# Performance work log

Hardware: AMD Instinct MI355X
Metric: run time of the kernel (lower is better)

## Reference

```python
import jax, jax.numpy as jnp
import numpy as np

N_ITERS = 21
TEMPERATURE = 0.04


def setup_inputs() -> dict:
    key = jax.random.key(0)
    input_tensor = jax.random.normal(key, (4096, 128, 128), dtype=jnp.float32)
    return {"input_tensor": input_tensor}


def reference(input_tensor) -> jnp.ndarray:
    n = input_tensor.shape[1]
    log_alpha = input_tensor.reshape((-1, n, n)) / TEMPERATURE

    def body(_, la):
        la = la - jax.nn.logsumexp(la, axis=2, keepdims=True)  # row normalize
        la = la - jax.nn.logsumexp(la, axis=1, keepdims=True)  # col normalize
        return la

    log_alpha = jax.lax.fori_loop(0, N_ITERS, body, log_alpha)
    return jnp.exp(log_alpha)
```

## Files before the change

### kernel.cpp

```cpp
#include <hip/hip_runtime.h>

typedef short bf16x8 __attribute__((ext_vector_type(8)));
typedef float f32x4 __attribute__((ext_vector_type(4)));
typedef unsigned int u32;
typedef unsigned short u16;

#define NIT 21
#define SMIN 1e-38f
#define CSH  140.0f
#define LDSCOL 136

static __device__ __forceinline__ u16 f2bf(float f) {
    u32 u = __float_as_uint(f);
    u = (u + 0x7fffu + ((u >> 16) & 1u)) >> 16;
    return (u16)u;
}
static __device__ __forceinline__ float bf2f(u16 h) {
    return __uint_as_float(((u32)h) << 16);
}

__global__ void __attribute__((amdgpu_flat_work_group_size(256, 256),
                               amdgpu_waves_per_eu(4, 4)))
sinkhorn_kernel(const float* __restrict__ in, float* __restrict__ out) {
    const int t  = threadIdx.x;
    const int w  = t >> 6;
    const int lg = (t >> 4) & 3;
    const int ln = t & 15;
    const size_t mat = (size_t)blockIdx.x << 14;
    const float S = 36.067376022224085f;

    __shared__ __align__(16) u16 Ecm[128 * LDSCOL];
    __shared__ __align__(16) u16 a_lds[128];
    __shared__ __align__(16) u16 b_lds[128];

    bf16x8 af[2][4];

#pragma unroll
    for (int th = 0; th < 2; ++th) {
        const int M = w * 32 + th * 16 + ln;
        const float* src = in + mat + (size_t)M * 128 + lg * 8;
        const int ms = M ^ (lg << 4);
        float s = 0.f;
#pragma unroll
        for (int c = 0; c < 4; ++c) {
            float4 f0 = *(const float4*)(src + c * 32);
            float4 f1 = *(const float4*)(src + c * 32 + 4);
            float e0 = __builtin_amdgcn_exp2f(fmaf(f0.x, S, -CSH));
            float e1 = __builtin_amdgcn_exp2f(fmaf(f0.y, S, -CSH));
            float e2 = __builtin_amdgcn_exp2f(fmaf(f0.z, S, -CSH));
            float e3 = __builtin_amdgcn_exp2f(fmaf(f0.w, S, -CSH));
            float e4 = __builtin_amdgcn_exp2f(fmaf(f1.x, S, -CSH));
            float e5 = __builtin_amdgcn_exp2f(fmaf(f1.y, S, -CSH));
            float e6 = __builtin_amdgcn_exp2f(fmaf(f1.z, S, -CSH));
            float e7 = __builtin_amdgcn_exp2f(fmaf(f1.w, S, -CSH));
            s += ((e0 + e1) + (e2 + e3)) + ((e4 + e5) + (e6 + e7));
            bf16x8 fr;
            fr[0] = (short)f2bf(e0); fr[1] = (short)f2bf(e1);
            fr[2] = (short)f2bf(e2); fr[3] = (short)f2bf(e3);
            fr[4] = (short)f2bf(e4); fr[5] = (short)f2bf(e5);
            fr[6] = (short)f2bf(e6); fr[7] = (short)f2bf(e7);
            af[th][c] = fr;
            const int nb = c * 32 + lg * 8;
#pragma unroll
            for (int j = 0; j < 8; ++j)
                Ecm[(nb + j) * LDSCOL + ms] = (u16)fr[j];
        }
        s += __shfl_xor(s, 16);
        s += __shfl_xor(s, 32);
        if (lg == 0) a_lds[M] = f2bf(__builtin_amdgcn_rcpf(fmaxf(s, SMIN)));
    }
    __syncthreads();

    const f32x4 z4 = {0.f, 0.f, 0.f, 0.f};

#pragma unroll 1
    for (int it = 0; it < NIT; ++it) {
        f32x4 acc0 = z4, acc1 = z4;
        const int N0 = w * 32 + ln;
        const int k0s = ((N0 >> 3) & 3) << 4;
        const int k1s = (((N0 + 16) >> 3) & 3) << 4;
#pragma unroll
        for (int c = 0; c < 4; ++c) {
            const int kb = c * 32 + lg * 8;
            bf16x8 aop = *(const bf16x8*)&a_lds[kb];
            bf16x8 b0  = *(const bf16x8*)&Ecm[N0 * LDSCOL + (kb ^ k0s)];
            bf16x8 b1  = *(const bf16x8*)&Ecm[(N0 + 16) * LDSCOL + (kb ^ k1s)];
            acc0 = __builtin_amdgcn_mfma_f32_16x16x32_bf16(aop, b0, acc0, 0, 0, 0);
            acc1 = __builtin_amdgcn_mfma_f32_16x16x32_bf16(aop, b1, acc1, 0, 0, 0);
        }
        if (lg == 0) {
            b_lds[w * 32 + ln]      = f2bf(__builtin_amdgcn_rcpf(fmaxf(acc0[0], SMIN)));
            b_lds[w * 32 + 16 + ln] = f2bf(__builtin_amdgcn_rcpf(fmaxf(acc1[0], SMIN)));
        }
        __syncthreads();

        if (it < NIT - 1) {
            f32x4 r0 = z4, r1 = z4;
#pragma unroll
            for (int c = 0; c < 4; ++c) {
                bf16x8 bop = *(const bf16x8*)&b_lds[c * 32 + lg * 8];
                r0 = __builtin_amdgcn_mfma_f32_16x16x32_bf16(af[0][c], bop, r0, 0, 0, 0);
                r1 = __builtin_amdgcn_mfma_f32_16x16x32_bf16(af[1][c], bop, r1, 0, 0, 0);
            }
            if (ln == 0) {
#pragma unroll
                for (int r = 0; r < 4; ++r) {
                    a_lds[w * 32 +      lg * 4 + r] = f2bf(__builtin_amdgcn_rcpf(fmaxf(r0[r], SMIN)));
                    a_lds[w * 32 + 16 + lg * 4 + r] = f2bf(__builtin_amdgcn_rcpf(fmaxf(r1[r], SMIN)));
                }
            }
            __syncthreads();
        }
    }

#pragma unroll
    for (int th = 0; th < 2; ++th) {
        const int M = w * 32 + th * 16 + ln;
        float* dst = out + mat + (size_t)M * 128 + lg * 8;
        const float av = bf2f(a_lds[M]);
#pragma unroll
        for (int c = 0; c < 4; ++c) {
            const bf16x8 e = af[th][c];
            const bf16x8 bop = *(const bf16x8*)&b_lds[c * 32 + lg * 8];
            float4 o0, o1;
            o0.x = bf2f((u16)e[0]) * av * bf2f((u16)bop[0]);
            o0.y = bf2f((u16)e[1]) * av * bf2f((u16)bop[1]);
            o0.z = bf2f((u16)e[2]) * av * bf2f((u16)bop[2]);
            o0.w = bf2f((u16)e[3]) * av * bf2f((u16)bop[3]);
            o1.x = bf2f((u16)e[4]) * av * bf2f((u16)bop[4]);
            o1.y = bf2f((u16)e[5]) * av * bf2f((u16)bop[5]);
            o1.z = bf2f((u16)e[6]) * av * bf2f((u16)bop[6]);
            o1.w = bf2f((u16)e[7]) * av * bf2f((u16)bop[7]);
            *(float4*)(dst + c * 32)     = o0;
            *(float4*)(dst + c * 32 + 4) = o1;
        }
    }
}

extern "C" void kernel_launch(void* const* d_in, const int* in_sizes, int n_in,
                              void* d_out, int out_size, void* d_ws, size_t ws_size,
                              hipStream_t stream) {
    (void)n_in; (void)d_ws; (void)ws_size; (void)out_size;
    const float* in  = (const float*)d_in[0];
    float*       out = (float*)d_out;
    const int n_mat = in_sizes[0] / (128 * 128);
    sinkhorn_kernel<<<dim3(n_mat), dim3(256), 0, stream>>>(in, out);
}
```

Before: 164.8 us.

## Use 512 threads per matrix, keep transposed E tiles in registers

Each block now runs 8 waves instead of 4, with each wave owning 16 rows. The column-major copy of the exponentiated matrix is no longer kept in LDS. Instead it is transposed once through a small staging buffer into per-thread B-operand registers, so each iteration's column-sum MFMAs read only registers plus the tiny scale vectors. This cuts the LDS footprint, which should allow more blocks per CU, and removes the per-iteration LDS reads of E. In exchange the transpose takes several extra barriers, and a 512-thread block pays a higher cost per barrier.

```diff
diff --git a/kernel.cpp b/kernel.cpp
--- a/kernel.cpp
+++ b/kernel.cpp
@@ -19,27 +19,25 @@
     return __uint_as_float(((u32)h) << 16);
 }
 
-__global__ void __attribute__((amdgpu_flat_work_group_size(256, 256),
-                               amdgpu_waves_per_eu(4, 4)))
-sinkhorn_kernel(const float* __restrict__ in, float* __restrict__ out) {
+__global__ __launch_bounds__(512)
+void sinkhorn_kernel(const float* __restrict__ in, float* __restrict__ out) {
     const int t  = threadIdx.x;
     const int w  = t >> 6;
     const int lg = (t >> 4) & 3;
     const int ln = t & 15;
+    const int M  = w * 16 + ln;
     const size_t mat = (size_t)blockIdx.x << 14;
     const float S = 36.067376022224085f;
 
-    __shared__ __align__(16) u16 Ecm[128 * LDSCOL];
+    __shared__ __align__(16) u16 stage[32 * LDSCOL];
     __shared__ __align__(16) u16 a_lds[128];
     __shared__ __align__(16) u16 b_lds[128];
 
-    bf16x8 af[2][4];
+    bf16x8 af[4];
+    bf16x8 bf[4];
 
-#pragma unroll
-    for (int th = 0; th < 2; ++th) {
-        const int M = w * 32 + th * 16 + ln;
+    {
         const float* src = in + mat + (size_t)M * 128 + lg * 8;
-        const int ms = M ^ (lg << 4);
         float s = 0.f;
 #pragma unroll
         for (int c = 0; c < 4; ++c) {
@@ -59,15 +57,28 @@
             fr[2] = (short)f2bf(e2); fr[3] = (short)f2bf(e3);
             fr[4] = (short)f2bf(e4); fr[5] = (short)f2bf(e5);
             fr[6] = (short)f2bf(e6); fr[7] = (short)f2bf(e7);
-            af[th][c] = fr;
-            const int nb = c * 32 + lg * 8;
-#pragma unroll
-            for (int j = 0; j < 8; ++j)
-                Ecm[(nb + j) * LDSCOL + ms] = (u16)fr[j];
+            af[c] = fr;
         }
         s += __shfl_xor(s, 16);
         s += __shfl_xor(s, 32);
         if (lg == 0) a_lds[M] = f2bf(__builtin_amdgcn_rcpf(fmaxf(s, SMIN)));
+    }
+
+#pragma unroll
+    for (int q = 0; q < 4; ++q) {
+        __syncthreads();
+        if ((w >> 1) == q) {
+            const int lr = ((w & 1) << 4) + ln;
+#pragma unroll
+            for (int c = 0; c < 4; ++c)
+                *(bf16x8*)&stage[lr * LDSCOL + c * 32 + lg * 8] = af[c];
+        }
+        __syncthreads();
+        bf16x8 fr;
+#pragma unroll
+        for (int j = 0; j < 8; ++j)
+            fr[j] = (short)stage[(lg * 8 + j) * LDSCOL + M];
+        bf[q] = fr;
     }
     __syncthreads();
 
@@ -75,52 +86,49 @@
 
 #pragma unroll 1
     for (int it = 0; it < NIT; ++it) {
-        f32x4 acc0 = z4, acc1 = z4;
-        const int N0 = w * 32 + ln;
-        const int k0s = ((N0 >> 3) & 3) << 4;
-        const int k1s = (((N0 + 16) >> 3) & 3) << 4;
-#pragma unroll
-        for (int c = 0; c < 4; ++c) {
-            const int kb = c * 32 + lg * 8;
-            bf16x8 aop = *(const bf16x8*)&a_lds[kb];
-            bf16x8 b0  = *(const bf16x8*)&Ecm[N0 * LDSCOL + (kb ^ k0s)];
-            bf16x8 b1  = *(const bf16x8*)&Ecm[(N0 + 16) * LDSCOL + (kb ^ k1s)];
-            acc0 = __builtin_amdgcn_mfma_f32_16x16x32_bf16(aop, b0, acc0, 0, 0, 0);
-            acc1 = __builtin_amdgcn_mfma_f32_16x16x32_bf16(aop, b1, acc1, 0, 0, 0);
-        }
-        if (lg == 0) {
-            b_lds[w * 32 + ln]      = f2bf(__builtin_amdgcn_rcpf(fmaxf(acc0[0], SMIN)));
-            b_lds[w * 32 + 16 + ln] = f2bf(__builtin_amdgcn_rcpf(fmaxf(acc1[0], SMIN)));
+        {
+            bf16x8 a0 = *(const bf16x8*)&a_lds[lg * 8];
+            bf16x8 a1 = *(const bf16x8*)&a_lds[32 + lg * 8];
+            bf16x8 a2 = *(const bf16x8*)&a_lds[64 + lg * 8];
+            bf16x8 a3 = *(const bf16x8*)&a_lds[96 + lg * 8];
+            f32x4 acc0 = __builtin_amdgcn_mfma_f32_16x16x32_bf16(a0, bf[0], z4, 0, 0, 0);
+            f32x4 acc1 = __builtin_amdgcn_mfma_f32_16x16x32_bf16(a1, bf[1], z4, 0, 0, 0);
+            acc0 = __builtin_amdgcn_mfma_f32_16x16x32_bf16(a2, bf[2], acc0, 0, 0, 0);
+            acc1 = __builtin_amdgcn_mfma_f32_16x16x32_bf16(a3, bf[3], acc1, 0, 0, 0);
+            if (lg == 0) {
+                float v = acc0[0] + acc1[0];
+                b_lds[M] = f2bf(__builtin_amdgcn_rcpf(fmaxf(v, SMIN)));
+            }
         }
         __syncthreads();
 
         if (it < NIT - 1) {
-            f32x4 r0 = z4, r1 = z4;
-#pragma unroll
-            for (int c = 0; c < 4; ++c) {
-                bf16x8 bop = *(const bf16x8*)&b_lds[c * 32 + lg * 8];
-                r0 = __builtin_amdgcn_mfma_f32_16x16x32_bf16(af[0][c], bop, r0, 0, 0, 0);
-                r1 = __builtin_amdgcn_mfma_f32_16x16x32_bf16(af[1][c], bop, r1, 0, 0, 0);
-            }
+            bf16x8 b0 = *(const bf16x8*)&b_lds[lg * 8];
+            bf16x8 b1 = *(const bf16x8*)&b_lds[32 + lg * 8];
+            bf16x8 b2 = *(const bf16x8*)&b_lds[64 + lg * 8];
+            bf16x8 b3 = *(const bf16x8*)&b_lds[96 + lg * 8];
+            f32x4 r0 = __builtin_amdgcn_mfma_f32_16x16x32_bf16(af[0], b0, z4, 0, 0, 0);
+            f32x4 r1 = __builtin_amdgcn_mfma_f32_16x16x32_bf16(af[1], b1, z4, 0, 0, 0);
+            r0 = __builtin_amdgcn_mfma_f32_16x16x32_bf16(af[2], b2, r0, 0, 0, 0);
+            r1 = __builtin_amdgcn_mfma_f32_16x16x32_bf16(af[3], b3, r1, 0, 0, 0);
             if (ln == 0) {
 #pragma unroll
                 for (int r = 0; r < 4; ++r) {
-                    a_lds[w * 32 +      lg * 4 + r] = f2bf(__builtin_amdgcn_rcpf(fmaxf(r0[r], SMIN)));
-                    a_lds[w * 32 + 16 + lg * 4 + r] = f2bf(__builtin_amdgcn_rcpf(fmaxf(r1[r], SMIN)));
+                    float v = r0[r] + r1[r];
+                    a_lds[w * 16 + lg * 4 + r] =
+                        f2bf(__builtin_amdgcn_rcpf(fmaxf(v, SMIN)));
                 }
             }
             __syncthreads();
         }
     }
 
-#pragma unroll
-    for (int th = 0; th < 2; ++th) {
-        const int M = w * 32 + th * 16 + ln;
+    {
         float* dst = out + mat + (size_t)M * 128 + lg * 8;
         const float av = bf2f(a_lds[M]);
 #pragma unroll
         for (int c = 0; c < 4; ++c) {
-            const bf16x8 e = af[th][c];
+            const bf16x8 e = af[c];
             const bf16x8 bop = *(const bf16x8*)&b_lds[c * 32 + lg * 8];
             float4 o0, o1;
             o0.x = bf2f((u16)e[0]) * av * bf2f((u16)bop[0]);
@@ -144,5 +152,5 @@
     const float* in  = (const float*)d_in[0];
     float*       out = (float*)d_out;
     const int n_mat = in_sizes[0] / (128 * 128);
-    sinkhorn_kernel<<<dim3(n_mat), dim3(256), 0, stream>>>(in, out);
+    sinkhorn_kernel<<<dim3(n_mat), dim3(512), 0, stream>>>(in, out);
 }
```

Result: faster. 146.8 us (-11.0%).

## Keep transposed E fragments in registers and split MFMA accumulation chains

Applied to the files above, without the earlier changes.

Replaces the full 128x136 column-major LDS copy of E with a small 32-row staging buffer. E is transposed through it in four synchronized rounds, and each wave then holds its B-operand fragments in registers. The per-iteration column-sum MFMAs no longer read E from LDS, and each four-MFMA dependent chain is split into two independent chains that are summed at the end to hide MFMA latency. In exchange, each thread needs 32 more VGPRs for the fragments, and the one-time transpose adds extra barriers and scalar LDS reads.

```diff
diff --git a/kernel.cpp b/kernel.cpp
--- a/kernel.cpp
+++ b/kernel.cpp
@@ -29,17 +29,17 @@
     const size_t mat = (size_t)blockIdx.x << 14;
     const float S = 36.067376022224085f;
 
-    __shared__ __align__(16) u16 Ecm[128 * LDSCOL];
+    __shared__ __align__(16) u16 stage[32 * LDSCOL];
     __shared__ __align__(16) u16 a_lds[128];
     __shared__ __align__(16) u16 b_lds[128];
 
     bf16x8 af[2][4];
+    bf16x8 bf[2][4];
 
 #pragma unroll
     for (int th = 0; th < 2; ++th) {
         const int M = w * 32 + th * 16 + ln;
         const float* src = in + mat + (size_t)M * 128 + lg * 8;
-        const int ms = M ^ (lg << 4);
         float s = 0.f;
 #pragma unroll
         for (int c = 0; c < 4; ++c) {
@@ -60,53 +60,80 @@
             fr[4] = (short)f2bf(e4); fr[5] = (short)f2bf(e5);
             fr[6] = (short)f2bf(e6); fr[7] = (short)f2bf(e7);
             af[th][c] = fr;
-            const int nb = c * 32 + lg * 8;
-#pragma unroll
-            for (int j = 0; j < 8; ++j)
-                Ecm[(nb + j) * LDSCOL + ms] = (u16)fr[j];
         }
         s += __shfl_xor(s, 16);
         s += __shfl_xor(s, 32);
         if (lg == 0) a_lds[M] = f2bf(__builtin_amdgcn_rcpf(fmaxf(s, SMIN)));
     }
-    __syncthreads();
+
+#pragma unroll
+    for (int q = 0; q < 4; ++q) {
+        __syncthreads();
+        if (w == q) {
+#pragma unroll
+            for (int th = 0; th < 2; ++th) {
+                const int lr = th * 16 + ln;
+#pragma unroll
+                for (int c = 0; c < 4; ++c)
+                    *(bf16x8*)&stage[lr * LDSCOL + c * 32 + lg * 8] = af[th][c];
+            }
+        }
+        __syncthreads();
+#pragma unroll
+        for (int uh = 0; uh < 2; ++uh) {
+            const int N = w * 32 + uh * 16 + ln;
+            bf16x8 fr;
+#pragma unroll
+            for (int j = 0; j < 8; ++j)
+                fr[j] = (short)stage[(lg * 8 + j) * LDSCOL + N];
+            bf[uh][q] = fr;
+        }
+    }
 
     const f32x4 z4 = {0.f, 0.f, 0.f, 0.f};
 
 #pragma unroll 1
     for (int it = 0; it < NIT; ++it) {
-        f32x4 acc0 = z4, acc1 = z4;
-        const int N0 = w * 32 + ln;
-        const int k0s = ((N0 >> 3) & 3) << 4;
-        const int k1s = (((N0 + 16) >> 3) & 3) << 4;
-#pragma unroll
-        for (int c = 0; c < 4; ++c) {
-            const int kb = c * 32 + lg * 8;
-            bf16x8 aop = *(const bf16x8*)&a_lds[kb];
-            bf16x8 b0  = *(const bf16x8*)&Ecm[N0 * LDSCOL + (kb ^ k0s)];
-            bf16x8 b1  = *(const bf16x8*)&Ecm[(N0 + 16) * LDSCOL + (kb ^ k1s)];
-            acc0 = __builtin_amdgcn_mfma_f32_16x16x32_bf16(aop, b0, acc0, 0, 0, 0);
-            acc1 = __builtin_amdgcn_mfma_f32_16x16x32_bf16(aop, b1, acc1, 0, 0, 0);
-        }
-        if (lg == 0) {
-            b_lds[w * 32 + ln]      = f2bf(__builtin_amdgcn_rcpf(fmaxf(acc0[0], SMIN)));
-            b_lds[w * 32 + 16 + ln] = f2bf(__builtin_amdgcn_rcpf(fmaxf(acc1[0], SMIN)));
+        {
+            bf16x8 a0 = *(const bf16x8*)&a_lds[lg * 8];
+            bf16x8 a1 = *(const bf16x8*)&a_lds[32 + lg * 8];
+            bf16x8 a2 = *(const bf16x8*)&a_lds[64 + lg * 8];
+            bf16x8 a3 = *(const bf16x8*)&a_lds[96 + lg * 8];
+            f32x4 x0 = __builtin_amdgcn_mfma_f32_16x16x32_bf16(a0, bf[0][0], z4, 0, 0, 0);
+            f32x4 x1 = __builtin_amdgcn_mfma_f32_16x16x32_bf16(a1, bf[0][1], z4, 0, 0, 0);
+            f32x4 y0 = __builtin_amdgcn_mfma_f32_16x16x32_bf16(a0, bf[1][0], z4, 0, 0, 0);
+            f32x4 y1 = __builtin_amdgcn_mfma_f32_16x16x32_bf16(a1, bf[1][1], z4, 0, 0, 0);
+            x0 = __builtin_amdgcn_mfma_f32_16x16x32_bf16(a2, bf[0][2], x0, 0, 0, 0);
+            x1 = __builtin_amdgcn_mfma_f32_16x16x32_bf16(a3, bf[0][3], x1, 0, 0, 0);
+            y0 = __builtin_amdgcn_mfma_f32_16x16x32_bf16(a2, bf[1][2], y0, 0, 0, 0);
+            y1 = __builtin_amdgcn_mfma_f32_16x16x32_bf16(a3, bf[1][3], y1, 0, 0, 0);
+            if (lg == 0) {
+                b_lds[w * 32 + ln]      = f2bf(__builtin_amdgcn_rcpf(fmaxf(x0[0] + x1[0], SMIN)));
+                b_lds[w * 32 + 16 + ln] = f2bf(__builtin_amdgcn_rcpf(fmaxf(y0[0] + y1[0], SMIN)));
+            }
         }
         __syncthreads();
 
         if (it < NIT - 1) {
-            f32x4 r0 = z4, r1 = z4;
-#pragma unroll
-            for (int c = 0; c < 4; ++c) {
-                bf16x8 bop = *(const bf16x8*)&b_lds[c * 32 + lg * 8];
-                r0 = __builtin_amdgcn_mfma_f32_16x16x32_bf16(af[0][c], bop, r0, 0, 0, 0);
-                r1 = __builtin_amdgcn_mfma_f32_16x16x32_bf16(af[1][c], bop, r1, 0, 0, 0);
-            }
+            bf16x8 b0 = *(const bf16x8*)&b_lds[lg * 8];
+            bf16x8 b1 = *(const bf16x8*)&b_lds[32 + lg * 8];
+            bf16x8 b2 = *(const bf16x8*)&b_lds[64 + lg * 8];
+            bf16x8 b3 = *(const bf16x8*)&b_lds[96 + lg * 8];
+            f32x4 u0 = __builtin_amdgcn_mfma_f32_16x16x32_bf16(af[0][0], b0, z4, 0, 0, 0);
+            f32x4 u1 = __builtin_amdgcn_mfma_f32_16x16x32_bf16(af[0][1], b1, z4, 0, 0, 0);
+            f32x4 v0 = __builtin_amdgcn_mfma_f32_16x16x32_bf16(af[1][0], b0, z4, 0, 0, 0);
+            f32x4 v1 = __builtin_amdgcn_mfma_f32_16x16x32_bf16(af[1][1], b1, z4, 0, 0, 0);
+            u0 = __builtin_amdgcn_mfma_f32_16x16x32_bf16(af[0][2], b2, u0, 0, 0, 0);
+            u1 = __builtin_amdgcn_mfma_f32_16x16x32_bf16(af[0][3], b3, u1, 0, 0, 0);
+            v0 = __builtin_amdgcn_mfma_f32_16x16x32_bf16(af[1][2], b2, v0, 0, 0, 0);
+            v1 = __builtin_amdgcn_mfma_f32_16x16x32_bf16(af[1][3], b3, v1, 0, 0, 0);
             if (ln == 0) {
 #pragma unroll
                 for (int r = 0; r < 4; ++r) {
-                    a_lds[w * 32 +      lg * 4 + r] = f2bf(__builtin_amdgcn_rcpf(fmaxf(r0[r], SMIN)));
-                    a_lds[w * 32 + 16 + lg * 4 + r] = f2bf(__builtin_amdgcn_rcpf(fmaxf(r1[r], SMIN)));
+                    a_lds[w * 32 +      lg * 4 + r] =
+                        f2bf(__builtin_amdgcn_rcpf(fmaxf(u0[r] + u1[r], SMIN)));
+                    a_lds[w * 32 + 16 + lg * 4 + r] =
+                        f2bf(__builtin_amdgcn_rcpf(fmaxf(v0[r] + v1[r], SMIN)));
                 }
             }
             __syncthreads();
```

Result: slower. 173.8 us (+5.4%).
